# Kernel optimization log

Hardware: AMD Instinct MI355X
Metric: run time of the kernel (lower is better)

The kernel has to match this reference:

```python
import jax, jax.numpy as jnp
import numpy as np

B, N, C = 32, 4096, 768
H = 24              # 2 * n_heads per MAPBlock
D = C // H          # head dim = 32
HID = 4 * C         # mlp hidden = 3072
EPS = 1e-6


def _rms_norm(x, w):
    # RMSNorm: x * rsqrt(mean(x^2)) * w
    return x * jax.lax.rsqrt(jnp.mean(x * x, axis=-1, keepdims=True) + EPS) * w


def setup_inputs() -> dict:
    key = jax.random.key(0)
    ks = jax.random.split(key, 12)
    s = 0.02
    return {
        "x": jax.random.normal(ks[0], (B, N, C), jnp.float32),
        "init_embed": jax.random.normal(ks[1], (B, C), jnp.float32),
        "latents": jax.random.normal(ks[2], (1, C), jnp.float32) * s,
        "proj_w": jax.random.normal(ks[3], (C, C), jnp.float32) * s,
        "proj_b": jnp.zeros((C,), jnp.float32),
        "q_w": jax.random.normal(ks[4], (C, C), jnp.float32) * s,
        "kv_w": jax.random.normal(ks[5], (C, 2 * C), jnp.float32) * s,
        "attn_o_w": jax.random.normal(ks[6], (C, C), jnp.float32) * s,
        "attn_o_b": jnp.zeros((C,), jnp.float32),
        "attn_norm_w": jnp.ones((C,), jnp.float32),
        "mlp_norm_w": jnp.ones((C,), jnp.float32),
        "glu_w": jax.random.normal(ks[7], (C, 2 * HID), jnp.float32) * s,
        "glu_b": jnp.zeros((2 * HID,), jnp.float32),
        "mlp_out_w": jax.random.normal(ks[8], (HID, C), jnp.float32) * s,
        "mlp_out_b": jnp.zeros((C,), jnp.float32),
    }


def reference(x, init_embed, latents, proj_w, proj_b, q_w, kv_w, attn_o_w,
              attn_o_b, attn_norm_w, mlp_norm_w, glu_w, glu_b, mlp_out_w,
              mlp_out_b):
    Bx = x.shape[0]
    K = latents.shape[0]
    scale = D ** -0.5

    # broadcast latents + init_embed -> [B, K, C]
    lat = latents[None, :, :] + init_embed[:, None, :]

    # input projection of pooled tokens
    xp = x @ proj_w + proj_b                                  # [B, N, C]

    # cross-attention: latents query the projected tokens
    q = (lat @ q_w).reshape(Bx, K, H, D)                      # [B, K, H, D]
    kv = (xp @ kv_w).reshape(Bx, N, 2, H, D)
    k, v = kv[:, :, 0], kv[:, :, 1]                           # [B, N, H, D]
    scores = jnp.einsum('bkhd,bnhd->bhkn', q, k) * scale      # [B, H, K, N]
    attn = jax.nn.softmax(scores, axis=-1)
    vals = jnp.einsum('bhkn,bnhd->bkhd', attn, v).reshape(Bx, K, C)
    attn_out = vals @ attn_o_w + attn_o_b                     # [B, K, C]

    # post-norm residual (attention)
    lat = _rms_norm(lat + attn_out, attn_norm_w)

    # SwishGLU MLP: projected * silu(gate)
    h = lat @ glu_w + glu_b                                   # [B, K, 2*HID]
    projected, gate = h[..., :HID], h[..., HID:]
    mlp = (projected * jax.nn.silu(gate)) @ mlp_out_w + mlp_out_b

    # post-norm residual (MLP)
    lat = _rms_norm(lat + mlp, mlp_norm_w)
    return jnp.squeeze(lat, axis=1)                           # [B, C] (K == 1)
```

## Files before the change

kernel.cpp:

```cpp
#include <hip/hip_runtime.h>
#include <math.h>

#define BB 32
#define NN 4096
#define CC 768
#define HH 24
#define HID 3072
#define N2 1536
#define EPSV 1e-6f
#define SCALE 0.17677669529663687f

#define SLICE_S  ((size_t)BB*HH*NN)
#define SLICE_P  ((size_t)BB*HH*CC)

#define OFF_WF     0
#define OFF_Q      (OFF_WF   + CC*N2)
#define OFF_WQ     (OFF_Q    + BB*CC)
#define OFF_S      (OFF_WQ   + BB*HH*CC)
#define OFF_PPART  (OFF_S    + 2*BB*HH*NN)
#define OFF_POOL   (OFF_PPART+ 32*BB*HH*CC)
#define OFF_MLP    (OFF_POOL + BB*HH*CC)
#define OFF_KVB    (OFF_MLP  + BB*CC)
#define OFF_HBUF   (OFF_KVB  + N2)
#define OFF_VPART  (OFF_HBUF + BB*2*HID)
#define OFF_VALS   (OFF_VPART+ 8*BB*CC)
#define OFF_OPART  (OFF_VALS + BB*CC)
#define OFF_LAT2   (OFF_OPART+ 8*BB*CC)
#define OFF_MLPIN  (OFF_LAT2 + BB*CC)
#define ZERO_START OFF_MLP
#define ZERO_FLOATS (BB*CC + N2 + BB*2*HID)

__global__ void wf_gemm(const float* __restrict__ A, const float* __restrict__ Bm,
                        float* __restrict__ Wf) {
    __shared__ float As[32][34];
    __shared__ float Bs[32][68];
    int t = threadIdx.x;
    int tx = t & 15, ty = t >> 4;
    int n0 = blockIdx.x * 64, m0 = blockIdx.y * 32;
    int ar = t >> 3, ak4 = t & 7;
    int bk = t >> 4, bn4 = t & 15;
    const float* Ap  = &A[(size_t)(m0 + ar) * 768 + ak4 * 4];
    const float* Bp0 = &Bm[(size_t)bk * 1536 + n0 + bn4 * 4];
    const float* Bp1 = &Bm[(size_t)(bk + 16) * 1536 + n0 + bn4 * 4];
    float4 a_reg  = *(const float4*)Ap;
    float4 b_reg0 = *(const float4*)Bp0;
    float4 b_reg1 = *(const float4*)Bp1;
    float acc[2][4] = {};
    for (int kt = 0; kt < 24; ++kt) {
        __syncthreads();
        As[ak4 * 4 + 0][ar] = a_reg.x;
        As[ak4 * 4 + 1][ar] = a_reg.y;
        As[ak4 * 4 + 2][ar] = a_reg.z;
        As[ak4 * 4 + 3][ar] = a_reg.w;
        *(float4*)&Bs[bk][bn4 * 4]      = b_reg0;
        *(float4*)&Bs[bk + 16][bn4 * 4] = b_reg1;
        __syncthreads();
        if (kt < 23) {
            int k0 = (kt + 1) * 32;
            a_reg  = *(const float4*)(Ap + k0);
            b_reg0 = *(const float4*)(Bp0 + (size_t)k0 * 1536);
            b_reg1 = *(const float4*)(Bp1 + (size_t)k0 * 1536);
        }
        #pragma unroll
        for (int kk = 0; kk < 32; ++kk) {
            float a0 = As[kk][ty * 2], a1 = As[kk][ty * 2 + 1];
            float4 bv = *(const float4*)&Bs[kk][tx * 4];
            acc[0][0] += a0 * bv.x; acc[0][1] += a0 * bv.y;
            acc[0][2] += a0 * bv.z; acc[0][3] += a0 * bv.w;
            acc[1][0] += a1 * bv.x; acc[1][1] += a1 * bv.y;
            acc[1][2] += a1 * bv.z; acc[1][3] += a1 * bv.w;
        }
    }
    #pragma unroll
    for (int i = 0; i < 2; ++i) {
        int m = m0 + ty * 2 + i;
        *(float4*)&Wf[(size_t)m * 1536 + n0 + tx * 4] =
            make_float4(acc[i][0], acc[i][1], acc[i][2], acc[i][3]);
    }
}

__global__ void kvbias_k(const float* __restrict__ pb, const float* __restrict__ kvw,
                         float* __restrict__ kvb) {
    int j = 768 + blockIdx.x * 256 + threadIdx.x;
    int i0 = blockIdx.y * 192;
    float acc = 0.f;
    for (int i = i0; i < i0 + 192; ++i) acc += pb[i] * kvw[(size_t)i * 1536 + j];
    atomicAdd(&kvb[j], acc);
}

__global__ void q_k(const float* __restrict__ latents, const float* __restrict__ emb,
                    const float* __restrict__ qw, float* __restrict__ q) {
    __shared__ float Ls[768];
    int b = blockIdx.y, t = threadIdx.x;
    for (int i = t; i < 768; i += 256) Ls[i] = latents[i] + emb[b * 768 + i];
    __syncthreads();
    int j = blockIdx.x * 256 + t;
    float acc = 0.f;
    for (int c = 0; c < 768; ++c) acc += Ls[c] * qw[c * 768 + j];
    q[b * 768 + j] = acc;
}

__global__ void wq_k(const float* __restrict__ Wf, const float* __restrict__ q,
                     float* __restrict__ wqT) {
    int h = blockIdx.x, b = blockIdx.y, t = threadIdx.x;
    __shared__ float qh[32];
    if (t < 32) qh[t] = q[b * 768 + h * 32 + t];
    __syncthreads();
    for (int c = t; c < 768; c += 256) {
        const float4* wrow = (const float4*)&Wf[(size_t)c * 1536 + h * 32];
        float acc = 0.f;
        #pragma unroll
        for (int d4 = 0; d4 < 8; ++d4) {
            float4 w = wrow[d4];
            acc += w.x * qh[4*d4] + w.y * qh[4*d4+1] + w.z * qh[4*d4+2] + w.w * qh[4*d4+3];
        }
        wqT[((size_t)b * 768 + c) * 24 + h] = SCALE * acc;
    }
}

__global__ void scores_k(const float* __restrict__ x, const float* __restrict__ wqT,
                         float* __restrict__ Spart) {
    __shared__ float Xs[4][64][33];
    int b = blockIdx.z, cs = blockIdx.y;
    int t = threadIdx.x;
    int w = t >> 6, lane = t & 63;
    int n0 = blockIdx.x * 256 + w * 64;
    int sr = lane >> 3, sc = (lane & 7) * 4;
    const float* __restrict__ xbase = &x[((size_t)b * 4096 + n0) * 768 + cs * 384];
    const float* __restrict__ wb = &wqT[((size_t)b * 768 + cs * 384) * 24];
    float (*Xw)[33] = Xs[w];
    float acc[24];
    #pragma unroll
    for (int h = 0; h < 24; ++h) acc[h] = 0.f;
    float4 pf[8];
    #pragma unroll
    for (int it = 0; it < 8; ++it)
        pf[it] = *(const float4*)&xbase[(size_t)(sr + 8 * it) * 768 + sc];
    for (int ck = 0; ck < 12; ++ck) {
        #pragma unroll
        for (int it = 0; it < 8; ++it) {
            int r = sr + 8 * it;
            Xw[r][sc + 0] = pf[it].x; Xw[r][sc + 1] = pf[it].y;
            Xw[r][sc + 2] = pf[it].z; Xw[r][sc + 3] = pf[it].w;
        }
        if (ck < 11) {
            #pragma unroll
            for (int it = 0; it < 8; ++it)
                pf[it] = *(const float4*)&xbase[(size_t)(sr + 8 * it) * 768 + (ck + 1) * 32 + sc];
        }
        const float* __restrict__ wc = &wb[ck * 32 * 24];
        #pragma unroll
        for (int cc = 0; cc < 32; ++cc) {
            float xv = Xw[lane][cc];
            #pragma unroll
            for (int h = 0; h < 24; ++h)
                acc[h] += xv * wc[cc * 24 + h];
        }
    }
    int n = n0 + lane;
    #pragma unroll
    for (int h = 0; h < 24; ++h)
        Spart[((size_t)(cs * 32 + b) * 24 + h) * 4096 + n] = acc[h];
}

__global__ void softmax_k(float* __restrict__ Sp) {
    int row = blockIdx.x;
    int t = threadIdx.x;
    size_t base = (size_t)row * 4096;
    float v[16];
    float m = -1e30f;
    #pragma unroll
    for (int i = 0; i < 16; ++i) {
        int idx = t + 256 * i;
        v[i] = Sp[base + idx] + Sp[SLICE_S + base + idx];
        m = fmaxf(m, v[i]);
    }
    __shared__ float redm[4];
    for (int off = 32; off > 0; off >>= 1) m = fmaxf(m, __shfl_down(m, off));
    if ((t & 63) == 0) redm[t >> 6] = m;
    __syncthreads();
    m = fmaxf(fmaxf(redm[0], redm[1]), fmaxf(redm[2], redm[3]));
    float s = 0.f;
    #pragma unroll
    for (int i = 0; i < 16; ++i) { v[i] = __expf(v[i] - m); s += v[i]; }
    __shared__ float reds[4];
    for (int off = 32; off > 0; off >>= 1) s += __shfl_down(s, off);
    if ((t & 63) == 0) reds[t >> 6] = s;
    __syncthreads();
    s = reds[0] + reds[1] + reds[2] + reds[3];
    float inv = 1.0f / s;
    #pragma unroll
    for (int i = 0; i < 16; ++i) Sp[base + t + 256 * i] = v[i] * inv;
}

__global__ void pooled_k(const float* __restrict__ x, const float* __restrict__ S,
                         float* __restrict__ ppart) {
    int nt = blockIdx.x, b = blockIdx.y;
    int t = threadIdx.x;
    int c = t * 4;
    int n0 = nt * 128;
    const float* __restrict__ Sb = &S[(size_t)b * 24 * 4096 + n0];
    const float* __restrict__ xb = &x[((size_t)b * 4096 + n0) * 768 + c];
    float ax[24], ay[24], az[24], aw[24];
    #pragma unroll
    for (int h = 0; h < 24; ++h) { ax[h]=0.f; ay[h]=0.f; az[h]=0.f; aw[h]=0.f; }
    #pragma unroll 4
    for (int i = 0; i < 128; ++i) {
        float4 xv = *(const float4*)&xb[(size_t)i * 768];
        #pragma unroll
        for (int h = 0; h < 24; ++h) {
            float s = Sb[h * 4096 + i];
            ax[h] += s * xv.x; ay[h] += s * xv.y;
            az[h] += s * xv.z; aw[h] += s * xv.w;
        }
    }
    float* dst = &ppart[(size_t)(nt * 32 + b) * 24 * 768];
    #pragma unroll
    for (int h = 0; h < 24; ++h)
        *(float4*)&dst[h * 768 + c] = make_float4(ax[h], ay[h], az[h], aw[h]);
}

__global__ void reduce_k(const float* __restrict__ ppart, float* __restrict__ pool) {
    size_t base = ((size_t)blockIdx.x * 256 + threadIdx.x) * 4;
    float sx=0.f, sy=0.f, sz=0.f, sw=0.f;
    #pragma unroll 8
    for (int sl = 0; sl < 32; ++sl) {
        float4 v = *(const float4*)&ppart[(size_t)sl * SLICE_P + base];
        sx += v.x; sy += v.y; sz += v.z; sw += v.w;
    }
    *(float4*)&pool[base] = make_float4(sx, sy, sz, sw);
}

__global__ void vals_k(const float* __restrict__ pool, const float* __restrict__ Wf,
                       float* __restrict__ vpart) {
    __shared__ float Ls[24][96];
    int b = blockIdx.x, cs = blockIdx.y, t = threadIdx.x;
    int c0 = cs * 96;
    for (int idx = t; idx < 24 * 96; idx += 768) {
        int hh = idx / 96, cc = idx % 96;
        Ls[hh][cc] = pool[((size_t)b * 24 + hh) * 768 + c0 + cc];
    }
    __syncthreads();
    int h = t >> 5;
    float acc = 0.f;
    for (int cc = 0; cc < 96; ++cc)
        acc += Ls[h][cc] * Wf[(size_t)(c0 + cc) * 1536 + 768 + t];
    vpart[((size_t)cs * 32 + b) * 768 + t] = acc;
}

__global__ void valsfin_k(const float* __restrict__ vpart, const float* __restrict__ kvb,
                          float* __restrict__ vals) {
    int b = blockIdx.x, t = threadIdx.x;
    float v = kvb[768 + t];
    #pragma unroll
    for (int cs = 0; cs < 8; ++cs) v += vpart[((size_t)cs * 32 + b) * 768 + t];
    vals[b * 768 + t] = v;
}

__global__ void oproj_k(const float* __restrict__ vals, const float* __restrict__ ow,
                        float* __restrict__ opart) {
    __shared__ float Vs[96];
    int b = blockIdx.x, cs = blockIdx.y, t = threadIdx.x;
    int c0 = cs * 96;
    if (t < 96) Vs[t] = vals[b * 768 + c0 + t];
    __syncthreads();
    float acc = 0.f;
    for (int cc = 0; cc < 96; ++cc)
        acc += Vs[cc] * ow[(size_t)(c0 + cc) * 768 + t];
    opart[((size_t)cs * 32 + b) * 768 + t] = acc;
}

__global__ void attnfin_k(const float* __restrict__ opart, const float* __restrict__ ob,
                          const float* __restrict__ latents, const float* __restrict__ emb,
                          const float* __restrict__ nw, float* __restrict__ lat2) {
    int b = blockIdx.x, t = threadIdx.x;
    float y = latents[t] + emb[b * 768 + t] + ob[t];
    #pragma unroll
    for (int cs = 0; cs < 8; ++cs) y += opart[((size_t)cs * 32 + b) * 768 + t];
    float s = y * y;
    for (int off = 32; off > 0; off >>= 1) s += __shfl_down(s, off);
    __shared__ float red[12];
    if ((t & 63) == 0) red[t >> 6] = s;
    __syncthreads();
    float tot = 0.f;
    #pragma unroll
    for (int w = 0; w < 12; ++w) tot += red[w];
    float rstd = rsqrtf(tot / 768.0f + EPSV);
    lat2[b * 768 + t] = y * rstd * nw[t];
}

__global__ void glu_k(const float* __restrict__ lat2, const float* __restrict__ gw,
                      const float* __restrict__ gb, float* __restrict__ hbuf) {
    int jt = blockIdx.x, bg = blockIdx.y, cs = blockIdx.z, t = threadIdx.x;
    int j = jt * 256 + t;
    float accP[4] = {0.f,0.f,0.f,0.f}, accG[4] = {0.f,0.f,0.f,0.f};
    if (cs == 0) {
        float bp = gb[j], bgv = gb[j + 3072];
        #pragma unroll
        for (int bb = 0; bb < 4; ++bb) { accP[bb] = bp; accG[bb] = bgv; }
    }
    const float* __restrict__ l2 = &lat2[(size_t)(bg * 4) * 768 + cs * 256];
    for (int c = 0; c < 256; ++c) {
        float wp = gw[(size_t)(cs * 256 + c) * 6144 + j];
        float wg = gw[(size_t)(cs * 256 + c) * 6144 + 3072 + j];
        #pragma unroll
        for (int bb = 0; bb < 4; ++bb) {
            float lv = l2[bb * 768 + c];
            accP[bb] += lv * wp;
            accG[bb] += lv * wg;
        }
    }
    #pragma unroll
    for (int bb = 0; bb < 4; ++bb) {
        atomicAdd(&hbuf[(size_t)(bg * 4 + bb) * 6144 + j],        accP[bb]);
        atomicAdd(&hbuf[(size_t)(bg * 4 + bb) * 6144 + 3072 + j], accG[bb]);
    }
}

__global__ void gfin_k(const float* __restrict__ hbuf, float* __restrict__ mlpin) {
    int idx = blockIdx.x * 256 + threadIdx.x;
    int b = idx / 3072, j = idx % 3072;
    float P = hbuf[(size_t)b * 6144 + j];
    float G = hbuf[(size_t)b * 6144 + 3072 + j];
    mlpin[idx] = P * (G / (1.0f + __expf(-G)));
}

__global__ void mlpout_k(const float* __restrict__ mlpin, const float* __restrict__ mw,
                         const float* __restrict__ mb, float* __restrict__ mlp) {
    int jt = blockIdx.x, bg = blockIdx.y, ic = blockIdx.z, t = threadIdx.x;
    int j = jt * 256 + t;
    int i0 = ic * 384;
    const float* __restrict__ mi = &mlpin[(size_t)(bg * 4) * 3072 + i0];
    float acc[4] = {0.f, 0.f, 0.f, 0.f};
    for (int i = 0; i < 384; ++i) {
        float w = mw[(size_t)(i0 + i) * 768 + j];
        #pragma unroll
        for (int bb = 0; bb < 4; ++bb)
            acc[bb] += mi[bb * 3072 + i] * w;
    }
    float bias = (ic == 0) ? mb[j] : 0.f;
    #pragma unroll
    for (int bb = 0; bb < 4; ++bb)
        atomicAdd(&mlp[(bg * 4 + bb) * 768 + j], acc[bb] + bias);
}

__global__ void fnorm_k(const float* __restrict__ lat2, const float* __restrict__ mlp,
                        const float* __restrict__ nw, float* __restrict__ out) {
    int b = blockIdx.x, t = threadIdx.x;
    float y = lat2[b * 768 + t] + mlp[b * 768 + t];
    float s = y * y;
    for (int off = 32; off > 0; off >>= 1) s += __shfl_down(s, off);
    __shared__ float red[12];
    if ((t & 63) == 0) red[t >> 6] = s;
    __syncthreads();
    float tot = 0.f;
    #pragma unroll
    for (int w = 0; w < 12; ++w) tot += red[w];
    float rstd = rsqrtf(tot / 768.0f + EPSV);
    out[b * 768 + t] = y * rstd * nw[t];
}

extern "C" void kernel_launch(void* const* d_in, const int* in_sizes, int n_in,
                              void* d_out, int out_size, void* d_ws, size_t ws_size,
                              hipStream_t stream) {
    const float* x       = (const float*)d_in[0];
    const float* emb     = (const float*)d_in[1];
    const float* latents = (const float*)d_in[2];
    const float* proj_w  = (const float*)d_in[3];
    const float* proj_b  = (const float*)d_in[4];
    const float* q_w     = (const float*)d_in[5];
    const float* kv_w    = (const float*)d_in[6];
    const float* ao_w    = (const float*)d_in[7];
    const float* ao_b    = (const float*)d_in[8];
    const float* anw     = (const float*)d_in[9];
    const float* mnw     = (const float*)d_in[10];
    const float* glu_w   = (const float*)d_in[11];
    const float* glu_b   = (const float*)d_in[12];
    const float* mo_w    = (const float*)d_in[13];
    const float* mo_b    = (const float*)d_in[14];

    float* ws    = (float*)d_ws;
    float* Wf    = ws + OFF_WF;
    float* q     = ws + OFF_Q;
    float* wqT   = ws + OFF_WQ;
    float* Sp    = ws + OFF_S;
    float* ppart = ws + OFF_PPART;
    float* pool  = ws + OFF_POOL;
    float* mlp   = ws + OFF_MLP;
    float* kvb   = ws + OFF_KVB;
    float* hbuf  = ws + OFF_HBUF;
    float* vpart = ws + OFF_VPART;
    float* vals  = ws + OFF_VALS;
    float* opart = ws + OFF_OPART;
    float* lat2  = ws + OFF_LAT2;
    float* mlpin = ws + OFF_MLPIN;

    hipMemsetAsync(ws + ZERO_START, 0, (size_t)ZERO_FLOATS * sizeof(float), stream);

    wf_gemm<<<dim3(24, 24), 256, 0, stream>>>(proj_w, kv_w, Wf);
    kvbias_k<<<dim3(3, 4), 256, 0, stream>>>(proj_b, kv_w, kvb);
    q_k<<<dim3(3, 32), 256, 0, stream>>>(latents, emb, q_w, q);
    wq_k<<<dim3(24, 32), 256, 0, stream>>>(Wf, q, wqT);

    scores_k<<<dim3(16, 2, 32), 256, 0, stream>>>(x, wqT, Sp);
    softmax_k<<<dim3(768), 256, 0, stream>>>(Sp);
    pooled_k<<<dim3(32, 32), 192, 0, stream>>>(x, Sp, ppart);
    reduce_k<<<dim3(576), 256, 0, stream>>>(ppart, pool);

    vals_k<<<dim3(32, 8), 768, 0, stream>>>(pool, Wf, vpart);
    valsfin_k<<<dim3(32), 768, 0, stream>>>(vpart, kvb, vals);
    oproj_k<<<dim3(32, 8), 768, 0, stream>>>(vals, ao_w, opart);
    attnfin_k<<<dim3(32), 768, 0, stream>>>(opart, ao_b, latents, emb, anw, lat2);

    glu_k<<<dim3(12, 8, 3), 256, 0, stream>>>(lat2, glu_w, glu_b, hbuf);
    gfin_k<<<dim3(384), 256, 0, stream>>>(hbuf, mlpin);
    mlpout_k<<<dim3(3, 8, 8), 256, 0, stream>>>(mlpin, mo_w, mo_b, mlp);
    fnorm_k<<<dim3(32), 768, 0, stream>>>(lat2, mlp, mnw, (float*)d_out);
}
```

Before: 461.5 us.

## Fuse kv-bias into weight GEMM, atomically reduce pooled partials, fold vals finalize

Computes the projected kv bias inside the weight-fusion GEMM's first row of blocks, removing the separate bias kernel. The pooled kernel now accumulates its 32 token-tile partials straight into the pool buffer with float atomics, so the 75 MB partial buffer and its reduce kernel go away. The pool buffer is zeroed in the existing memset instead. The vals finalize step is folded into the output-projection kernel's load. This cuts kernel launches and global traffic, at the cost of atomic contention and a non-deterministic summation order.

```diff
diff --git a/kernel.cpp b/kernel.cpp
--- a/kernel.cpp
+++ b/kernel.cpp
@@ -11,32 +11,33 @@
 #define SCALE 0.17677669529663687f
 
 #define SLICE_S  ((size_t)BB*HH*NN)
-#define SLICE_P  ((size_t)BB*HH*CC)
 
 #define OFF_WF     0
 #define OFF_Q      (OFF_WF   + CC*N2)
 #define OFF_WQ     (OFF_Q    + BB*CC)
 #define OFF_S      (OFF_WQ   + BB*HH*CC)
-#define OFF_PPART  (OFF_S    + 2*BB*HH*NN)
-#define OFF_POOL   (OFF_PPART+ 32*BB*HH*CC)
+#define OFF_POOL   (OFF_S    + 2*BB*HH*NN)
 #define OFF_MLP    (OFF_POOL + BB*HH*CC)
 #define OFF_KVB    (OFF_MLP  + BB*CC)
 #define OFF_HBUF   (OFF_KVB  + N2)
 #define OFF_VPART  (OFF_HBUF + BB*2*HID)
-#define OFF_VALS   (OFF_VPART+ 8*BB*CC)
-#define OFF_OPART  (OFF_VALS + BB*CC)
+#define OFF_OPART  (OFF_VPART+ 8*BB*CC)
 #define OFF_LAT2   (OFF_OPART+ 8*BB*CC)
 #define OFF_MLPIN  (OFF_LAT2 + BB*CC)
-#define ZERO_START OFF_MLP
-#define ZERO_FLOATS (BB*CC + N2 + BB*2*HID)
+#define ZERO_START OFF_POOL
+#define ZERO_FLOATS (BB*HH*CC + BB*CC + N2 + BB*2*HID)
 
 __global__ void wf_gemm(const float* __restrict__ A, const float* __restrict__ Bm,
-                        float* __restrict__ Wf) {
+                        const float* __restrict__ pb, float* __restrict__ Wf,
+                        float* __restrict__ kvb) {
     __shared__ float As[32][34];
     __shared__ float Bs[32][68];
+    __shared__ float pbs[768];
     int t = threadIdx.x;
     int tx = t & 15, ty = t >> 4;
     int n0 = blockIdx.x * 64, m0 = blockIdx.y * 32;
+    bool doBias = (blockIdx.y == 0);
+    if (doBias) for (int i = t; i < 768; i += 256) pbs[i] = pb[i];
     int ar = t >> 3, ak4 = t & 7;
     int bk = t >> 4, bn4 = t & 15;
     const float* Ap  = &A[(size_t)(m0 + ar) * 768 + ak4 * 4];
@@ -46,6 +47,7 @@
     float4 b_reg0 = *(const float4*)Bp0;
     float4 b_reg1 = *(const float4*)Bp1;
     float acc[2][4] = {};
+    float bacc[4] = {0.f, 0.f, 0.f, 0.f};
     for (int kt = 0; kt < 24; ++kt) {
         __syncthreads();
         As[ak4 * 4 + 0][ar] = a_reg.x;
@@ -70,6 +72,16 @@
             acc[1][0] += a1 * bv.x; acc[1][1] += a1 * bv.y;
             acc[1][2] += a1 * bv.z; acc[1][3] += a1 * bv.w;
         }
+        if (doBias && ty == 0) {
+            int kbase = kt * 32;
+            #pragma unroll
+            for (int kk = 0; kk < 32; ++kk) {
+                float p = pbs[kbase + kk];
+                float4 bv = *(const float4*)&Bs[kk][tx * 4];
+                bacc[0] += p * bv.x; bacc[1] += p * bv.y;
+                bacc[2] += p * bv.z; bacc[3] += p * bv.w;
+            }
+        }
     }
     #pragma unroll
     for (int i = 0; i < 2; ++i) {
@@ -77,15 +89,8 @@
         *(float4*)&Wf[(size_t)m * 1536 + n0 + tx * 4] =
             make_float4(acc[i][0], acc[i][1], acc[i][2], acc[i][3]);
     }
-}
-
-__global__ void kvbias_k(const float* __restrict__ pb, const float* __restrict__ kvw,
-                         float* __restrict__ kvb) {
-    int j = 768 + blockIdx.x * 256 + threadIdx.x;
-    int i0 = blockIdx.y * 192;
-    float acc = 0.f;
-    for (int i = i0; i < i0 + 192; ++i) acc += pb[i] * kvw[(size_t)i * 1536 + j];
-    atomicAdd(&kvb[j], acc);
+    if (doBias && ty == 0)
+        *(float4*)&kvb[n0 + tx * 4] = make_float4(bacc[0], bacc[1], bacc[2], bacc[3]);
 }
 
 __global__ void q_k(const float* __restrict__ latents, const float* __restrict__ emb,
@@ -194,7 +199,7 @@
 }
 
 __global__ void pooled_k(const float* __restrict__ x, const float* __restrict__ S,
-                         float* __restrict__ ppart) {
+                         float* __restrict__ pool) {
     int nt = blockIdx.x, b = blockIdx.y;
     int t = threadIdx.x;
     int c = t * 4;
@@ -214,21 +219,14 @@
             az[h] += s * xv.z; aw[h] += s * xv.w;
         }
     }
-    float* dst = &ppart[(size_t)(nt * 32 + b) * 24 * 768];
-    #pragma unroll
-    for (int h = 0; h < 24; ++h)
-        *(float4*)&dst[h * 768 + c] = make_float4(ax[h], ay[h], az[h], aw[h]);
-}
-
-__global__ void reduce_k(const float* __restrict__ ppart, float* __restrict__ pool) {
-    size_t base = ((size_t)blockIdx.x * 256 + threadIdx.x) * 4;
-    float sx=0.f, sy=0.f, sz=0.f, sw=0.f;
-    #pragma unroll 8
-    for (int sl = 0; sl < 32; ++sl) {
-        float4 v = *(const float4*)&ppart[(size_t)sl * SLICE_P + base];
-        sx += v.x; sy += v.y; sz += v.z; sw += v.w;
-    }
-    *(float4*)&pool[base] = make_float4(sx, sy, sz, sw);
+    float* dst = &pool[(size_t)b * 24 * 768];
+    #pragma unroll
+    for (int h = 0; h < 24; ++h) {
+        atomicAdd(&dst[h * 768 + c + 0], ax[h]);
+        atomicAdd(&dst[h * 768 + c + 1], ay[h]);
+        atomicAdd(&dst[h * 768 + c + 2], az[h]);
+        atomicAdd(&dst[h * 768 + c + 3], aw[h]);
+    }
 }
 
 __global__ void vals_k(const float* __restrict__ pool, const float* __restrict__ Wf,
@@ -248,21 +246,17 @@
     vpart[((size_t)cs * 32 + b) * 768 + t] = acc;
 }
 
-__global__ void valsfin_k(const float* __restrict__ vpart, const float* __restrict__ kvb,
-                          float* __restrict__ vals) {
-    int b = blockIdx.x, t = threadIdx.x;
-    float v = kvb[768 + t];
-    #pragma unroll
-    for (int cs = 0; cs < 8; ++cs) v += vpart[((size_t)cs * 32 + b) * 768 + t];
-    vals[b * 768 + t] = v;
-}
-
-__global__ void oproj_k(const float* __restrict__ vals, const float* __restrict__ ow,
-                        float* __restrict__ opart) {
+__global__ void oproj_k(const float* __restrict__ vpart, const float* __restrict__ kvb,
+                        const float* __restrict__ ow, float* __restrict__ opart) {
     __shared__ float Vs[96];
     int b = blockIdx.x, cs = blockIdx.y, t = threadIdx.x;
     int c0 = cs * 96;
-    if (t < 96) Vs[t] = vals[b * 768 + c0 + t];
+    if (t < 96) {
+        float v = kvb[768 + c0 + t];
+        #pragma unroll
+        for (int s2 = 0; s2 < 8; ++s2) v += vpart[((size_t)s2 * 32 + b) * 768 + c0 + t];
+        Vs[t] = v;
+    }
     __syncthreads();
     float acc = 0.f;
     for (int cc = 0; cc < 96; ++cc)
@@ -384,32 +378,27 @@
     float* q     = ws + OFF_Q;
     float* wqT   = ws + OFF_WQ;
     float* Sp    = ws + OFF_S;
-    float* ppart = ws + OFF_PPART;
     float* pool  = ws + OFF_POOL;
     float* mlp   = ws + OFF_MLP;
     float* kvb   = ws + OFF_KVB;
     float* hbuf  = ws + OFF_HBUF;
     float* vpart = ws + OFF_VPART;
-    float* vals  = ws + OFF_VALS;
     float* opart = ws + OFF_OPART;
     float* lat2  = ws + OFF_LAT2;
     float* mlpin = ws + OFF_MLPIN;
 
     hipMemsetAsync(ws + ZERO_START, 0, (size_t)ZERO_FLOATS * sizeof(float), stream);
 
-    wf_gemm<<<dim3(24, 24), 256, 0, stream>>>(proj_w, kv_w, Wf);
-    kvbias_k<<<dim3(3, 4), 256, 0, stream>>>(proj_b, kv_w, kvb);
+    wf_gemm<<<dim3(24, 24), 256, 0, stream>>>(proj_w, kv_w, proj_b, Wf, kvb);
     q_k<<<dim3(3, 32), 256, 0, stream>>>(latents, emb, q_w, q);
     wq_k<<<dim3(24, 32), 256, 0, stream>>>(Wf, q, wqT);
 
     scores_k<<<dim3(16, 2, 32), 256, 0, stream>>>(x, wqT, Sp);
     softmax_k<<<dim3(768), 256, 0, stream>>>(Sp);
-    pooled_k<<<dim3(32, 32), 192, 0, stream>>>(x, Sp, ppart);
-    reduce_k<<<dim3(576), 256, 0, stream>>>(ppart, pool);
+    pooled_k<<<dim3(32, 32), 192, 0, stream>>>(x, Sp, pool);
 
     vals_k<<<dim3(32, 8), 768, 0, stream>>>(pool, Wf, vpart);
-    valsfin_k<<<dim3(32), 768, 0, stream>>>(vpart, kvb, vals);
-    oproj_k<<<dim3(32, 8), 768, 0, stream>>>(vals, ao_w, opart);
+    oproj_k<<<dim3(32, 8), 768, 0, stream>>>(vpart, kvb, ao_w, opart);
     attnfin_k<<<dim3(32), 768, 0, stream>>>(opart, ao_b, latents, emb, anw, lat2);
 
     glu_k<<<dim3(12, 8, 3), 256, 0, stream>>>(lat2, glu_w, glu_b, hbuf);
```

Measured after the change: 1.263 ms. +173.6%, slower.
